# Optimization experiments

Measured on AMD Instinct MI355X. Metric: run time of the kernel, lower is better.

Reference implementation:

```python
import jax, jax.numpy as jnp
import numpy as np

LN_EPS = 1e-5

def _quantize(w):
    # round(W / mean|W|), clamp to {-1,0,1}, with straight-through estimator
    wq = jnp.clip(jnp.round(w / jnp.mean(jnp.abs(w))), -1.0, 1.0)
    return w + jax.lax.stop_gradient(wq - w)

def _ternary_linear(x, W, gamma, beta):
    mu = jnp.mean(x, axis=-1, keepdims=True)
    var = jnp.mean(jnp.square(x - mu), axis=-1, keepdims=True)
    xn = (x - mu) * jax.lax.rsqrt(var + LN_EPS) * gamma + beta
    return xn @ _quantize(W)

def setup_inputs() -> dict:
    key = jax.random.key(0)
    ks = jax.random.split(key, 10)
    B, T, E, H = 4, 4096, 1024, 64
    x = jax.random.normal(ks[0], (B, T, E), dtype=jnp.float32)
    Wk = jax.random.normal(ks[1], (E, H), dtype=jnp.float32)
    Wq = jax.random.normal(ks[2], (E, H), dtype=jnp.float32)
    Wv = jax.random.normal(ks[3], (E, H), dtype=jnp.float32)
    gk = jnp.ones((E,), jnp.float32); bk = jnp.zeros((E,), jnp.float32)
    gq = jnp.ones((E,), jnp.float32); bq = jnp.zeros((E,), jnp.float32)
    gv = jnp.ones((E,), jnp.float32); bv = jnp.zeros((E,), jnp.float32)
    return {"x": x, "Wk": Wk, "Wq": Wq, "Wv": Wv,
            "gk": gk, "bk": bk, "gq": gq, "bq": bq, "gv": gv, "bv": bv}

def reference(x, Wk, Wq, Wv, gk, bk, gq, bq, gv, bv):
    k = _ternary_linear(x, Wk, gk, bk)   # [B,T,H]
    q = _ternary_linear(x, Wq, gq, bq)   # [B,T,H]
    v = _ternary_linear(x, Wv, gv, bv)   # [B,T,H]
    scale = k.shape[-1] ** -0.5
    wei = jnp.einsum('bth,bsh->bts', q, k) * scale  # [B,T,T]
    wei = jax.nn.softmax(wei, axis=-1)              # dropout p=0 -> identity
    return jnp.einsum('bts,bsh->bth', wei, v)       # [B,T,H]
```

## Files before the change

### kernel.cpp

```cpp
#include <hip/hip_runtime.h>
#include <math.h>

#define LN_EPS 1e-5f

typedef __attribute__((ext_vector_type(8))) short    bf16x8;
typedef __attribute__((ext_vector_type(8))) _Float16 f16x8;
typedef __attribute__((ext_vector_type(4))) float    f32x4;

__device__ inline ushort f2bf(float f){
    union { float f; uint u; } v; v.f = f;
    uint r = v.u + 0x7fffu + ((v.u >> 16) & 1u);
    return (ushort)(r >> 16);
}
__device__ inline float bf2f(ushort h){
    union { uint u; float f; } v; v.u = ((uint)h) << 16;
    return v.f;
}
__device__ inline ushort f2h(float f){
    union { _Float16 h; ushort u; } v; v.h = (_Float16)f;
    return v.u;
}


__global__ __launch_bounds__(1024) void quant_k(
    const float* __restrict__ Wq, const float* __restrict__ Wk, const float* __restrict__ Wv,
    const float* __restrict__ gq, const float* __restrict__ bq,
    const float* __restrict__ gk, const float* __restrict__ bk,
    const float* __restrict__ gv, const float* __restrict__ bv,
    float* __restrict__ Wcat, float* __restrict__ cvec)
{
    const int br = blockIdx.x;
    const float* W = (br==0) ? Wq : (br==1 ? Wk : Wv);
    const float* g = (br==0) ? gq : (br==1 ? gk : gv);
    const float* bb= (br==0) ? bq : (br==1 ? bk : bv);
    const int t = threadIdx.x;
    __shared__ float red[1024];
    float s = 0.f;
    #pragma unroll 4
    for (int i=0;i<64;i++) s += fabsf(W[t + 1024*i]);
    red[t] = s;
    __syncthreads();
    for (int o=512;o>0;o>>=1){ if (t<o) red[t]+=red[t+o]; __syncthreads(); }
    const float mean = red[0] * (1.0f/65536.0f);

    const float ge = g[t];
    for (int h=0; h<64; h++) {
        float w  = W[t*64+h];
        float wq = fminf(1.f, fmaxf(-1.f, rintf(w/mean)));
        Wcat[t*192 + br*64 + h] = ge*wq;
    }
    const int h = t & 63, chunk = t >> 6;
    float cp = 0.f;
    for (int i=0;i<64;i++){
        int e = chunk*64 + i;
        float w  = W[e*64+h];
        float wq = fminf(1.f, fmaxf(-1.f, rintf(w/mean)));
        cp += bb[e]*wq;
    }
    __shared__ float cred[16][64];
    cred[chunk][h] = cp;
    __syncthreads();
    if (t < 64){
        float c = 0.f;
        #pragma unroll
        for (int i=0;i<16;i++) c += cred[i][t];
        cvec[br*64 + t] = c;
    }
}

__global__ __launch_bounds__(256) void lngemm_k(
    const float* __restrict__ x, const float* __restrict__ Wcat,
    const float* __restrict__ cvec, float* __restrict__ qf,
    ushort* __restrict__ khi, ushort* __restrict__ klo,
    ushort* __restrict__ vthi, ushort* __restrict__ vtlo)
{
    __shared__ float As[16][68];
    __shared__ float Bs[16][192];
    __shared__ float mu_s[64], rs_s[64];
    const int t  = threadIdx.x;
    const int r0 = blockIdx.x * 64;

    const int arow = t >> 2, apart = t & 3;
    const int bkk  = t >> 4, bn   = (t & 15) * 12;

    float4 aV = *(const float4*)(x + (r0 + arow)*1024 + apart*4);
    const float* wr0 = Wcat + bkk*192 + bn;
    float4 bV0 = *(const float4*)(wr0);
    float4 bV1 = *(const float4*)(wr0+4);
    float4 bV2 = *(const float4*)(wr0+8);

    {
        const float* xr = x + (r0 + arow)*1024 + apart*4;
        float s1=0.f, s2=0.f;
        #pragma unroll 8
        for (int j=0;j<64;j++){
            float4 v = *(const float4*)(xr + j*16);
            s1 += v.x+v.y+v.z+v.w;
            s2 += v.x*v.x+v.y*v.y+v.z*v.z+v.w*v.w;
        }
        s1 += __shfl_xor(s1,1); s1 += __shfl_xor(s1,2);
        s2 += __shfl_xor(s2,1); s2 += __shfl_xor(s2,2);
        if (apart==0){
            float mu  = s1*(1.f/1024.f);
            float var = s2*(1.f/1024.f) - mu*mu;
            mu_s[arow]=mu; rs_s[arow]=rsqrtf(var+LN_EPS);
        }
    }
    __syncthreads();
    const float mu = mu_s[arow], rs = rs_s[arow];

    const int tx = t & 15, ty = t >> 4;
    float4 c0 = *(const float4*)(cvec + tx*4);
    float4 c1 = *(const float4*)(cvec + tx*4 + 64);
    float4 c2 = *(const float4*)(cvec + tx*4 + 128);
    float4 acc[4][3];
    #pragma unroll
    for (int mi=0;mi<4;mi++){ acc[mi][0]=c0; acc[mi][1]=c1; acc[mi][2]=c2; }

    for (int kt=0; kt<64; kt++){
        As[apart*4+0][arow] = (aV.x-mu)*rs;
        As[apart*4+1][arow] = (aV.y-mu)*rs;
        As[apart*4+2][arow] = (aV.z-mu)*rs;
        As[apart*4+3][arow] = (aV.w-mu)*rs;
        *(float4*)&Bs[bkk][bn+0] = bV0;
        *(float4*)&Bs[bkk][bn+4] = bV1;
        *(float4*)&Bs[bkk][bn+8] = bV2;
        __syncthreads();
        if (kt < 63){
            aV = *(const float4*)(x + (r0 + arow)*1024 + (kt+1)*16 + apart*4);
            const float* wr = Wcat + ((kt+1)*16 + bkk)*192 + bn;
            bV0 = *(const float4*)(wr);
            bV1 = *(const float4*)(wr+4);
            bV2 = *(const float4*)(wr+8);
        }
        #pragma unroll
        for (int kk=0;kk<16;kk++){
            float4 a4  = *(const float4*)&As[kk][ty*4];
            float4 b40 = *(const float4*)&Bs[kk][tx*4];
            float4 b41 = *(const float4*)&Bs[kk][tx*4+64];
            float4 b42 = *(const float4*)&Bs[kk][tx*4+128];
            float am[4] = {a4.x, a4.y, a4.z, a4.w};
            #pragma unroll
            for (int mi=0;mi<4;mi++){
                acc[mi][0].x += am[mi]*b40.x; acc[mi][0].y += am[mi]*b40.y;
                acc[mi][0].z += am[mi]*b40.z; acc[mi][0].w += am[mi]*b40.w;
                acc[mi][1].x += am[mi]*b41.x; acc[mi][1].y += am[mi]*b41.y;
                acc[mi][1].z += am[mi]*b41.z; acc[mi][1].w += am[mi]*b41.w;
                acc[mi][2].x += am[mi]*b42.x; acc[mi][2].y += am[mi]*b42.y;
                acc[mi][2].z += am[mi]*b42.z; acc[mi][2].w += am[mi]*b42.w;
            }
        }
        __syncthreads();
    }
    #pragma unroll
    for (int mi=0;mi<4;mi++){
        const int grow = r0 + ty*4 + mi;
        *(float4*)(qf + grow*64 + tx*4) = acc[mi][0];
        float kf[4] = {acc[mi][1].x, acc[mi][1].y, acc[mi][1].z, acc[mi][1].w};
        uint2 uh, ul;
        {
            ushort h0=f2bf(kf[0]), h1=f2bf(kf[1]), h2=f2bf(kf[2]), h3=f2bf(kf[3]);
            ushort l0=f2h(kf[0]-bf2f(h0)), l1=f2h(kf[1]-bf2f(h1));
            ushort l2=f2h(kf[2]-bf2f(h2)), l3=f2h(kf[3]-bf2f(h3));
            uh.x = (uint)h0 | ((uint)h1<<16); uh.y = (uint)h2 | ((uint)h3<<16);
            ul.x = (uint)l0 | ((uint)l1<<16); ul.y = (uint)l2 | ((uint)l3<<16);
        }
        *(uint2*)(khi + (size_t)grow*64 + tx*4) = uh;
        *(uint2*)(klo + (size_t)grow*64 + tx*4) = ul;
        float vf[4] = {acc[mi][2].x, acc[mi][2].y, acc[mi][2].z, acc[mi][2].w};
        const int bb2 = grow >> 12, tt = grow & 4095;
        #pragma unroll
        for (int c=0;c<4;c++){
            int h = tx*4 + c;
            ushort hb = f2bf(vf[c]);
            vthi[((size_t)bb2*64 + h)*4096 + tt] = hb;
            vtlo[((size_t)bb2*64 + h)*4096 + tt] = f2bf(vf[c] - bf2f(hb));
        }
    }
}

__global__ __launch_bounds__(256, 2) void attn_mfma_k(
    const float* __restrict__ qf, const ushort* __restrict__ khi,
    const ushort* __restrict__ klo, const ushort* __restrict__ vthi,
    const ushort* __restrict__ vtlo, float* __restrict__ Opart,
    float* __restrict__ ml, int tps)
{
    __shared__ char smem[32768];

    const int t    = threadIdx.x;
    const int lane = t & 63;
    const int w    = t >> 6;
    const int lr   = lane & 15;
    const int lq   = lane >> 4;

    const int bid = blockIdx.x, nwg = gridDim.x;
    const int virt = (bid & 7) * (nwg >> 3) + (bid >> 3);
    const int ks = virt >> 8;
    const int b  = (virt >> 6) & 3;
    const int qt = virt & 63;

    const int gq = b*4096 + qt*64 + w*16 + lr;
    bf16x8 aqh[2]; f16x8 aqh16[2], aql16[2];
    #pragma unroll
    for (int ks2=0; ks2<2; ks2++){
        const float* qp = qf + (size_t)gq*64 + ks2*32 + lq*8;
        float4 qa = *(const float4*)(qp);
        float4 qb = *(const float4*)(qp+4);
        float qv[8] = {qa.x,qa.y,qa.z,qa.w,qb.x,qb.y,qb.z,qb.w};
        #pragma unroll
        for (int j=0;j<8;j++){
            float q = qv[j] * 0.125f;
            ushort hb = f2bf(q);
            float  hf = bf2f(hb);
            aqh[ks2][j]   = (short)hb;
            aqh16[ks2][j] = (_Float16)hf;
            aql16[ks2][j] = (_Float16)(q - hf);
        }
    }

    float m_[4], l_[4];
    f32x4 Oacc[4];
    #pragma unroll
    for (int i=0;i<4;i++){ m_[i] = -3.0e38f; l_[i] = 0.f; }
    #pragma unroll
    for (int n=0;n<4;n++) Oacc[n] = (f32x4){0.f,0.f,0.f,0.f};

    const int srow = t >> 2;
    const int sseg = (t & 3) * 32;
    const int sd0 = srow*128 + (sseg ^ ((srow&7)<<4));
    const int sd1 = srow*128 + ((sseg+16) ^ ((srow&7)<<4));

    for (int kt = ks*tps; kt < ks*tps + tps; kt++){
        __syncthreads();
        {
            const int grow = b*4096 + kt*64 + srow;
            const char* skh = (const char*)(khi + (size_t)grow*64) + sseg;
            const char* skl = (const char*)(klo + (size_t)grow*64) + sseg;
            const char* svh = (const char*)(vthi + ((size_t)b*64 + srow)*4096 + kt*64) + sseg;
            const char* svl = (const char*)(vtlo + ((size_t)b*64 + srow)*4096 + kt*64) + sseg;
            *(uint4*)(smem         + sd0) = *(const uint4*)(skh);
            *(uint4*)(smem         + sd1) = *(const uint4*)(skh+16);
            *(uint4*)(smem +  8192 + sd0) = *(const uint4*)(skl);
            *(uint4*)(smem +  8192 + sd1) = *(const uint4*)(skl+16);
            *(uint4*)(smem + 16384 + sd0) = *(const uint4*)(svh);
            *(uint4*)(smem + 16384 + sd1) = *(const uint4*)(svh+16);
            *(uint4*)(smem + 24576 + sd0) = *(const uint4*)(svl);
            *(uint4*)(smem + 24576 + sd1) = *(const uint4*)(svl+16);
        }
        __syncthreads();

        f32x4 sacc[4];
        #pragma unroll
        for (int n=0;n<4;n++) sacc[n] = (f32x4){0.f,0.f,0.f,0.f};
        #pragma unroll
        for (int ks2=0; ks2<2; ks2++){
            #pragma unroll
            for (int n=0;n<4;n++){
                const int row = n*16 + lr;
                const int bc  = (ks2*32 + lq*8)*2;
                const int off = row*128 + (bc ^ ((row&7)<<4));
                bf16x8 bkh = *(const bf16x8*)(smem + off);
                f16x8  bkl = *(const f16x8*)(smem + 8192 + off);
                f16x8  bkh16;
                #pragma unroll
                for (int j=0;j<8;j++) bkh16[j] = (_Float16)bf2f((ushort)bkh[j]);
                sacc[n] = __builtin_amdgcn_mfma_f32_16x16x32_bf16(aqh[ks2],  bkh,   sacc[n], 0,0,0);
                sacc[n] = __builtin_amdgcn_mfma_f32_16x16x32_f16 (aqh16[ks2], bkl,  sacc[n], 0,0,0);
                sacc[n] = __builtin_amdgcn_mfma_f32_16x16x32_f16 (aql16[ks2], bkh16,sacc[n], 0,0,0);
                sacc[n] = __builtin_amdgcn_mfma_f32_16x16x32_f16 (aql16[ks2], bkl,  sacc[n], 0,0,0);
            }
        }

        float pvals[4][4];
        float al[4];
        #pragma unroll
        for (int i=0;i<4;i++){
            float tm = fmaxf(fmaxf(sacc[0][i],sacc[1][i]), fmaxf(sacc[2][i],sacc[3][i]));
            tm = fmaxf(tm, __shfl_xor(tm,1));
            tm = fmaxf(tm, __shfl_xor(tm,2));
            tm = fmaxf(tm, __shfl_xor(tm,4));
            tm = fmaxf(tm, __shfl_xor(tm,8));
            float mn = fmaxf(m_[i], tm);
            float a  = __expf(m_[i] - mn);
            float rs = 0.f;
            #pragma unroll
            for (int n=0;n<4;n++){
                float p = __expf(sacc[n][i] - mn);
                pvals[n][i] = p;
                rs += p;
            }
            rs += __shfl_xor(rs,1);
            rs += __shfl_xor(rs,2);
            rs += __shfl_xor(rs,4);
            rs += __shfl_xor(rs,8);
            l_[i] = l_[i]*a + rs;
            m_[i] = mn;
            al[i] = a;
        }
        #pragma unroll
        for (int n=0;n<4;n++){
            #pragma unroll
            for (int i=0;i<4;i++) Oacc[n][i] *= al[i];
        }

        __syncthreads();
        char* Pw = smem + w*4096;
        #pragma unroll
        for (int n=0;n<4;n++){
            #pragma unroll
            for (int i=0;i<4;i++){
                const int row = lq*4 + i;
                const int bc  = (n*16 + lr)*4;
                float  p  = pvals[n][i];
                ushort ph = f2bf(p);
                ushort pl = f2bf(p - bf2f(ph));
                *(uint*)(Pw + row*256 + (bc ^ ((row&7)<<4))) = (uint)ph | ((uint)pl << 16);
            }
        }
        asm volatile("s_waitcnt lgkmcnt(0)" ::: "memory");

        #pragma unroll
        for (int ks2=0; ks2<2; ks2++){
            const int pbc = ks2*128 + lq*32;
            uint4 pv0 = *(const uint4*)(Pw + lr*256 + ( pbc      ^ ((lr&7)<<4)));
            uint4 pv1 = *(const uint4*)(Pw + lr*256 + ((pbc+16)  ^ ((lr&7)<<4)));
            uint pu[8] = {pv0.x,pv0.y,pv0.z,pv0.w,pv1.x,pv1.y,pv1.z,pv1.w};
            bf16x8 ph, pl;
            #pragma unroll
            for (int j=0;j<8;j++){
                ph[j] = (short)(pu[j] & 0xffffu);
                pl[j] = (short)(pu[j] >> 16);
            }
            #pragma unroll
            for (int n=0;n<4;n++){
                const int row = n*16 + lr;
                const int bc  = (ks2*32 + lq*8)*2;
                const int off = row*128 + (bc ^ ((row&7)<<4));
                bf16x8 bvh = *(const bf16x8*)(smem + 16384 + off);
                bf16x8 bvl = *(const bf16x8*)(smem + 24576 + off);
                Oacc[n] = __builtin_amdgcn_mfma_f32_16x16x32_bf16(ph, bvh, Oacc[n], 0,0,0);
                Oacc[n] = __builtin_amdgcn_mfma_f32_16x16x32_bf16(ph, bvl, Oacc[n], 0,0,0);
                Oacc[n] = __builtin_amdgcn_mfma_f32_16x16x32_bf16(pl, bvh, Oacc[n], 0,0,0);
            }
        }
    }

    #pragma unroll
    for (int n=0;n<4;n++){
        #pragma unroll
        for (int i=0;i<4;i++){
            const int row = b*4096 + qt*64 + w*16 + lq*4 + i;
            Opart[((size_t)ks*16384 + row)*64 + n*16 + lr] = Oacc[n][i];
        }
    }
    if (lr == 0){
        #pragma unroll
        for (int i=0;i<4;i++){
            const int row = b*4096 + qt*64 + w*16 + lq*4 + i;
            ml[((size_t)ks*16384 + row)*2 + 0] = m_[i];
            ml[((size_t)ks*16384 + row)*2 + 1] = l_[i];
        }
    }
}

__global__ __launch_bounds__(256) void combine_k(
    const float* __restrict__ Opart, const float* __restrict__ ml,
    float* __restrict__ out, int nsplit)
{
    const int t = threadIdx.x;
    const int tx = t & 15, ty = t >> 4;
    const int r = blockIdx.x * 16 + ty;
    float mstar = -3.0e38f;
    for (int s=0;s<nsplit;s++)
        mstar = fmaxf(mstar, ml[((size_t)s*16384 + r)*2]);
    float lstar = 0.f;
    float4 o = make_float4(0.f,0.f,0.f,0.f);
    for (int s=0;s<nsplit;s++){
        float ms = ml[((size_t)s*16384 + r)*2];
        float ls = ml[((size_t)s*16384 + r)*2 + 1];
        float wgt = __expf(ms - mstar);
        lstar += wgt * ls;
        float4 p = *(const float4*)(Opart + ((size_t)s*16384 + r)*64 + tx*4);
        o.x += wgt*p.x; o.y += wgt*p.y; o.z += wgt*p.z; o.w += wgt*p.w;
    }
    float inv = 1.0f / lstar;
    o.x*=inv; o.y*=inv; o.z*=inv; o.w*=inv;
    *(float4*)(out + (size_t)r*64 + tx*4) = o;
}

extern "C" void kernel_launch(void* const* d_in, const int* in_sizes, int n_in,
                              void* d_out, int out_size, void* d_ws, size_t ws_size,
                              hipStream_t stream) {
    const float* x  = (const float*)d_in[0];
    const float* Wk = (const float*)d_in[1];
    const float* Wq = (const float*)d_in[2];
    const float* Wv = (const float*)d_in[3];
    const float* gk = (const float*)d_in[4];
    const float* bk = (const float*)d_in[5];
    const float* gq = (const float*)d_in[6];
    const float* bq = (const float*)d_in[7];
    const float* gv = (const float*)d_in[8];
    const float* bv = (const float*)d_in[9];
    float* out = (float*)d_out;
    char* ws = (char*)d_ws;
    float*  Wcat = (float*)(ws);
    float*  cvec = (float*)(ws + 786432);
    float*  qf   = (float*)(ws + 1048576);
    ushort* khi  = (ushort*)(ws + 5242880);
    ushort* klo  = (ushort*)(ws + 7340032);
    ushort* vthi = (ushort*)(ws + 9437184);
    ushort* vtlo = (ushort*)(ws + 11534336);

    const size_t base = 13631488;
    int ns;
    if      (ws_size >= base + 4ull*4325376) ns = 4;
    else if (ws_size >= base + 2ull*4325376) ns = 2;
    else                                     ns = 1;
    float* Opart = (float*)(ws + base);
    float* mlp   = (float*)(ws + base + (size_t)ns*4194304);

    quant_k<<<dim3(3), dim3(1024), 0, stream>>>(Wq, Wk, Wv, gq, bq, gk, bk, gv, bv, Wcat, cvec);
    lngemm_k<<<dim3(256), dim3(256), 0, stream>>>(x, Wcat, cvec, qf, khi, klo, vthi, vtlo);
    attn_mfma_k<<<dim3(256*ns), dim3(256), 0, stream>>>(qf, khi, klo, vthi, vtlo, Opart, mlp, 64/ns);
    combine_k<<<dim3(1024), dim3(256), 0, stream>>>(Opart, mlp, out, ns);
}
```

Baseline: 360.6 us.

## Move LayerNorm-projection GEMM to bf16x3 MFMA with post-GEMM normalization

Result: faster. 326.0 us (-9.6%).

```diff
diff --git a/kernel.cpp b/kernel.cpp
--- a/kernel.cpp
+++ b/kernel.cpp
@@ -27,7 +27,8 @@
     const float* __restrict__ gq, const float* __restrict__ bq,
     const float* __restrict__ gk, const float* __restrict__ bk,
     const float* __restrict__ gv, const float* __restrict__ bv,
-    float* __restrict__ Wcat, float* __restrict__ cvec)
+    ushort* __restrict__ Wg_hi, ushort* __restrict__ Wg_lo,
+    float* __restrict__ colsumg, float* __restrict__ cvec)
 {
     const int br = blockIdx.x;
     const float* W = (br==0) ? Wq : (br==1 ? Wk : Wv);
@@ -47,50 +48,71 @@
     for (int h=0; h<64; h++) {
         float w  = W[t*64+h];
         float wq = fminf(1.f, fmaxf(-1.f, rintf(w/mean)));
-        Wcat[t*192 + br*64 + h] = ge*wq;
-    }
-    const int h = t & 63, chunk = t >> 6;
-    float cp = 0.f;
+        float wg = ge*wq;
+        ushort hh = f2bf(wg);
+        Wg_hi[(size_t)(br*64+h)*1024 + t] = hh;
+        Wg_lo[(size_t)(br*64+h)*1024 + t] = f2bf(wg - bf2f(hh));
+    }
+    const int h2 = t & 63, chunk = t >> 6;
+    float cg = 0.f, cb = 0.f;
     for (int i=0;i<64;i++){
         int e = chunk*64 + i;
-        float w  = W[e*64+h];
+        float w  = W[e*64+h2];
         float wq = fminf(1.f, fmaxf(-1.f, rintf(w/mean)));
-        cp += bb[e]*wq;
-    }
-    __shared__ float cred[16][64];
-    cred[chunk][h] = cp;
+        cg += g[e]*wq;
+        cb += bb[e]*wq;
+    }
+    __shared__ float credg[16][64];
+    __shared__ float credb[16][64];
+    credg[chunk][h2] = cg;
+    credb[chunk][h2] = cb;
     __syncthreads();
     if (t < 64){
-        float c = 0.f;
-        #pragma unroll
-        for (int i=0;i<16;i++) c += cred[i][t];
-        cvec[br*64 + t] = c;
+        float sg = 0.f, sb = 0.f;
+        #pragma unroll
+        for (int i=0;i<16;i++){ sg += credg[i][t]; sb += credb[i][t]; }
+        colsumg[br*64 + t] = sg;
+        cvec[br*64 + t]    = sb;
     }
 }
 
 __global__ __launch_bounds__(256) void lngemm_k(
-    const float* __restrict__ x, const float* __restrict__ Wcat,
+    const float* __restrict__ x, const ushort* __restrict__ Wg_hi,
+    const ushort* __restrict__ Wg_lo, const float* __restrict__ colsumg,
     const float* __restrict__ cvec, float* __restrict__ qf,
     ushort* __restrict__ khi, ushort* __restrict__ klo,
     ushort* __restrict__ vthi, ushort* __restrict__ vtlo)
 {
-    __shared__ float As[16][68];
-    __shared__ float Bs[16][192];
+    __shared__ char smem[65536];
     __shared__ float mu_s[64], rs_s[64];
+    char* Ah = smem;
+    char* Al = smem + 8192;
+    char* Bh = smem + 16384;
+    char* Bl = smem + 40960;
+
     const int t  = threadIdx.x;
     const int r0 = blockIdx.x * 64;
-
+    const int lane = t & 63, w = t >> 6, lr = lane & 15, lq = lane >> 4;
     const int arow = t >> 2, apart = t & 3;
-    const int bkk  = t >> 4, bn   = (t & 15) * 12;
-
-    float4 aV = *(const float4*)(x + (r0 + arow)*1024 + apart*4);
-    const float* wr0 = Wcat + bkk*192 + bn;
-    float4 bV0 = *(const float4*)(wr0);
-    float4 bV1 = *(const float4*)(wr0+4);
-    float4 bV2 = *(const float4*)(wr0+8);
-
+
+    float4 ax[4];
     {
-        const float* xr = x + (r0 + arow)*1024 + apart*4;
+        const float* xp = x + (size_t)(r0+arow)*1024 + apart*16;
+        ax[0]=*(const float4*)(xp);   ax[1]=*(const float4*)(xp+4);
+        ax[2]=*(const float4*)(xp+8); ax[3]=*(const float4*)(xp+12);
+    }
+    uint4 bhv[3][2], blv[3][2];
+    #pragma unroll
+    for (int cc=0;cc<3;cc++){
+        int id = cc*256 + t; int brow = id>>2; int bpart = id&3;
+        const ushort* ph = Wg_hi + (size_t)brow*1024 + bpart*16;
+        const ushort* pl = Wg_lo + (size_t)brow*1024 + bpart*16;
+        bhv[cc][0]=*(const uint4*)(ph); bhv[cc][1]=*(const uint4*)(ph+8);
+        blv[cc][0]=*(const uint4*)(pl); blv[cc][1]=*(const uint4*)(pl+8);
+    }
+
+    {
+        const float* xr = x + (size_t)(r0 + arow)*1024 + apart*4;
         float s1=0.f, s2=0.f;
         #pragma unroll 8
         for (int j=0;j<64;j++){
@@ -106,75 +128,99 @@
             mu_s[arow]=mu; rs_s[arow]=rsqrtf(var+LN_EPS);
         }
     }
-    __syncthreads();
-    const float mu = mu_s[arow], rs = rs_s[arow];
-
-    const int tx = t & 15, ty = t >> 4;
-    float4 c0 = *(const float4*)(cvec + tx*4);
-    float4 c1 = *(const float4*)(cvec + tx*4 + 64);
-    float4 c2 = *(const float4*)(cvec + tx*4 + 128);
-    float4 acc[4][3];
-    #pragma unroll
-    for (int mi=0;mi<4;mi++){ acc[mi][0]=c0; acc[mi][1]=c1; acc[mi][2]=c2; }
-
-    for (int kt=0; kt<64; kt++){
-        As[apart*4+0][arow] = (aV.x-mu)*rs;
-        As[apart*4+1][arow] = (aV.y-mu)*rs;
-        As[apart*4+2][arow] = (aV.z-mu)*rs;
-        As[apart*4+3][arow] = (aV.w-mu)*rs;
-        *(float4*)&Bs[bkk][bn+0] = bV0;
-        *(float4*)&Bs[bkk][bn+4] = bV1;
-        *(float4*)&Bs[bkk][bn+8] = bV2;
+
+    f32x4 acc[12];
+    #pragma unroll
+    for (int n=0;n<12;n++) acc[n] = (f32x4){0.f,0.f,0.f,0.f};
+
+    const int aswz = (arow&7)<<4;
+
+    for (int kt=0; kt<16; kt++){
+        {
+            float xs[16] = {ax[0].x,ax[0].y,ax[0].z,ax[0].w,
+                            ax[1].x,ax[1].y,ax[1].z,ax[1].w,
+                            ax[2].x,ax[2].y,ax[2].z,ax[2].w,
+                            ax[3].x,ax[3].y,ax[3].z,ax[3].w};
+            uint hu[8], lu[8];
+            #pragma unroll
+            for (int j=0;j<8;j++){
+                ushort h0 = f2bf(xs[2*j]),   h1 = f2bf(xs[2*j+1]);
+                ushort l0 = f2bf(xs[2*j]  - bf2f(h0));
+                ushort l1 = f2bf(xs[2*j+1]- bf2f(h1));
+                hu[j] = (uint)h0 | ((uint)h1<<16);
+                lu[j] = (uint)l0 | ((uint)l1<<16);
+            }
+            *(uint4*)(Ah + arow*128 + ((apart*32)    ^ aswz)) = (uint4){hu[0],hu[1],hu[2],hu[3]};
+            *(uint4*)(Ah + arow*128 + ((apart*32+16) ^ aswz)) = (uint4){hu[4],hu[5],hu[6],hu[7]};
+            *(uint4*)(Al + arow*128 + ((apart*32)    ^ aswz)) = (uint4){lu[0],lu[1],lu[2],lu[3]};
+            *(uint4*)(Al + arow*128 + ((apart*32+16) ^ aswz)) = (uint4){lu[4],lu[5],lu[6],lu[7]};
+            #pragma unroll
+            for (int cc=0;cc<3;cc++){
+                int id = cc*256 + t; int brow = id>>2; int bpart = id&3;
+                int bswz = (brow&7)<<4;
+                *(uint4*)(Bh + brow*128 + ((bpart*32)    ^ bswz)) = bhv[cc][0];
+                *(uint4*)(Bh + brow*128 + ((bpart*32+16) ^ bswz)) = bhv[cc][1];
+                *(uint4*)(Bl + brow*128 + ((bpart*32)    ^ bswz)) = blv[cc][0];
+                *(uint4*)(Bl + brow*128 + ((bpart*32+16) ^ bswz)) = blv[cc][1];
+            }
+        }
         __syncthreads();
-        if (kt < 63){
-            aV = *(const float4*)(x + (r0 + arow)*1024 + (kt+1)*16 + apart*4);
-            const float* wr = Wcat + ((kt+1)*16 + bkk)*192 + bn;
-            bV0 = *(const float4*)(wr);
-            bV1 = *(const float4*)(wr+4);
-            bV2 = *(const float4*)(wr+8);
-        }
-        #pragma unroll
-        for (int kk=0;kk<16;kk++){
-            float4 a4  = *(const float4*)&As[kk][ty*4];
-            float4 b40 = *(const float4*)&Bs[kk][tx*4];
-            float4 b41 = *(const float4*)&Bs[kk][tx*4+64];
-            float4 b42 = *(const float4*)&Bs[kk][tx*4+128];
-            float am[4] = {a4.x, a4.y, a4.z, a4.w};
-            #pragma unroll
-            for (int mi=0;mi<4;mi++){
-                acc[mi][0].x += am[mi]*b40.x; acc[mi][0].y += am[mi]*b40.y;
-                acc[mi][0].z += am[mi]*b40.z; acc[mi][0].w += am[mi]*b40.w;
-                acc[mi][1].x += am[mi]*b41.x; acc[mi][1].y += am[mi]*b41.y;
-                acc[mi][1].z += am[mi]*b41.z; acc[mi][1].w += am[mi]*b41.w;
-                acc[mi][2].x += am[mi]*b42.x; acc[mi][2].y += am[mi]*b42.y;
-                acc[mi][2].z += am[mi]*b42.z; acc[mi][2].w += am[mi]*b42.w;
+        if (kt < 15){
+            const float* xp = x + (size_t)(r0+arow)*1024 + (kt+1)*64 + apart*16;
+            ax[0]=*(const float4*)(xp);   ax[1]=*(const float4*)(xp+4);
+            ax[2]=*(const float4*)(xp+8); ax[3]=*(const float4*)(xp+12);
+            #pragma unroll
+            for (int cc=0;cc<3;cc++){
+                int id = cc*256 + t; int brow = id>>2; int bpart = id&3;
+                const ushort* ph = Wg_hi + (size_t)brow*1024 + (kt+1)*64 + bpart*16;
+                const ushort* pl = Wg_lo + (size_t)brow*1024 + (kt+1)*64 + bpart*16;
+                bhv[cc][0]=*(const uint4*)(ph); bhv[cc][1]=*(const uint4*)(ph+8);
+                blv[cc][0]=*(const uint4*)(pl); blv[cc][1]=*(const uint4*)(pl+8);
+            }
+        }
+        #pragma unroll
+        for (int kc=0;kc<2;kc++){
+            const int abc = kc*64 + lq*16;
+            const int ar  = w*16 + lr;
+            const int aoff = ar*128 + (abc ^ ((ar&7)<<4));
+            bf16x8 ah = *(const bf16x8*)(Ah + aoff);
+            bf16x8 al = *(const bf16x8*)(Al + aoff);
+            #pragma unroll
+            for (int n=0;n<12;n++){
+                const int br2 = n*16 + lr;
+                const int boff = br2*128 + (abc ^ ((br2&7)<<4));
+                bf16x8 bh = *(const bf16x8*)(Bh + boff);
+                bf16x8 bl = *(const bf16x8*)(Bl + boff);
+                acc[n] = __builtin_amdgcn_mfma_f32_16x16x32_bf16(ah, bh, acc[n], 0,0,0);
+                acc[n] = __builtin_amdgcn_mfma_f32_16x16x32_bf16(al, bh, acc[n], 0,0,0);
+                acc[n] = __builtin_amdgcn_mfma_f32_16x16x32_bf16(ah, bl, acc[n], 0,0,0);
             }
         }
         __syncthreads();
     }
-    #pragma unroll
-    for (int mi=0;mi<4;mi++){
-        const int grow = r0 + ty*4 + mi;
-        *(float4*)(qf + grow*64 + tx*4) = acc[mi][0];
-        float kf[4] = {acc[mi][1].x, acc[mi][1].y, acc[mi][1].z, acc[mi][1].w};
-        uint2 uh, ul;
-        {
-            ushort h0=f2bf(kf[0]), h1=f2bf(kf[1]), h2=f2bf(kf[2]), h3=f2bf(kf[3]);
-            ushort l0=f2h(kf[0]-bf2f(h0)), l1=f2h(kf[1]-bf2f(h1));
-            ushort l2=f2h(kf[2]-bf2f(h2)), l3=f2h(kf[3]-bf2f(h3));
-            uh.x = (uint)h0 | ((uint)h1<<16); uh.y = (uint)h2 | ((uint)h3<<16);
-            ul.x = (uint)l0 | ((uint)l1<<16); ul.y = (uint)l2 | ((uint)l3<<16);
-        }
-        *(uint2*)(khi + (size_t)grow*64 + tx*4) = uh;
-        *(uint2*)(klo + (size_t)grow*64 + tx*4) = ul;
-        float vf[4] = {acc[mi][2].x, acc[mi][2].y, acc[mi][2].z, acc[mi][2].w};
-        const int bb2 = grow >> 12, tt = grow & 4095;
-        #pragma unroll
-        for (int c=0;c<4;c++){
-            int h = tx*4 + c;
-            ushort hb = f2bf(vf[c]);
-            vthi[((size_t)bb2*64 + h)*4096 + tt] = hb;
-            vtlo[((size_t)bb2*64 + h)*4096 + tt] = f2bf(vf[c] - bf2f(hb));
+
+    #pragma unroll
+    for (int n=0;n<12;n++){
+        const int col = n*16 + lr;
+        const float csg = colsumg[col];
+        const float cv  = cvec[col];
+        #pragma unroll
+        for (int i=0;i<4;i++){
+            const int lrow = w*16 + lq*4 + i;
+            const int grow = r0 + lrow;
+            float val = rs_s[lrow]*(acc[n][i] - mu_s[lrow]*csg) + cv;
+            if (col < 64){
+                qf[(size_t)grow*64 + col] = val;
+            } else if (col < 128){
+                ushort hh = f2bf(val);
+                khi[(size_t)grow*64 + (col-64)] = hh;
+                klo[(size_t)grow*64 + (col-64)] = f2h(val - bf2f(hh));
+            } else {
+                const int b2 = grow >> 12, tt = grow & 4095, hcol = col - 128;
+                ushort hh = f2bf(val);
+                vthi[((size_t)b2*64 + hcol)*4096 + tt] = hh;
+                vtlo[((size_t)b2*64 + hcol)*4096 + tt] = f2bf(val - bf2f(hh));
+            }
         }
     }
 }
@@ -403,8 +449,10 @@
     const float* bv = (const float*)d_in[9];
     float* out = (float*)d_out;
     char* ws = (char*)d_ws;
-    float*  Wcat = (float*)(ws);
-    float*  cvec = (float*)(ws + 786432);
+    ushort* Wg_hi   = (ushort*)(ws);
+    ushort* Wg_lo   = (ushort*)(ws + 393216);
+    float*  colsumg = (float*)(ws + 786432);
+    float*  cvec    = (float*)(ws + 787200);
     float*  qf   = (float*)(ws + 1048576);
     ushort* khi  = (ushort*)(ws + 5242880);
     ushort* klo  = (ushort*)(ws + 7340032);
@@ -419,8 +467,10 @@
     float* Opart = (float*)(ws + base);
     float* mlp   = (float*)(ws + base + (size_t)ns*4194304);
 
-    quant_k<<<dim3(3), dim3(1024), 0, stream>>>(Wq, Wk, Wv, gq, bq, gk, bk, gv, bv, Wcat, cvec);
-    lngemm_k<<<dim3(256), dim3(256), 0, stream>>>(x, Wcat, cvec, qf, khi, klo, vthi, vtlo);
+    quant_k<<<dim3(3), dim3(1024), 0, stream>>>(Wq, Wk, Wv, gq, bq, gk, bk, gv, bv,
+                                                Wg_hi, Wg_lo, colsumg, cvec);
+    lngemm_k<<<dim3(256), dim3(256), 0, stream>>>(x, Wg_hi, Wg_lo, colsumg, cvec,
+                                                  qf, khi, klo, vthi, vtlo);
     attn_mfma_k<<<dim3(256*ns), dim3(256), 0, stream>>>(qf, khi, klo, vthi, vtlo, Opart, mlp, 64/ns);
     combine_k<<<dim3(1024), dim3(256), 0, stream>>>(Opart, mlp, out, ns);
 }
```
